# Performance work log

Hardware: AMD Instinct MI355X
Metric: run time of the kernel (lower is better)

The kernel has to match this reference:

```python
import jax, jax.numpy as jnp
import numpy as np

B, S, D, H = 2, 2048, 1024, 16
HD = D // H

def setup_inputs() -> dict:
    key = jax.random.key(0)
    k1, k2, k3 = jax.random.split(key, 3)
    x = jax.random.normal(k1, (B, S, D), dtype=jnp.float32)
    c_attn_w = jax.random.normal(k2, (D, 3 * D), dtype=jnp.float32) * 0.02
    c_attn_b = jnp.zeros((3 * D,), dtype=jnp.float32)
    c_proj_w = jax.random.normal(k3, (D, D), dtype=jnp.float32) * 0.02
    c_proj_b = jnp.zeros((D,), dtype=jnp.float32)
    return {"x": x, "c_attn_w": c_attn_w, "c_attn_b": c_attn_b,
            "c_proj_w": c_proj_w, "c_proj_b": c_proj_b}

def reference(x, c_attn_w, c_attn_b, c_proj_w, c_proj_b):
    bsz, seq_len, d = x.shape
    # Conv1D: addmm(bias, x, weight) -> x @ W + b
    qkv = x @ c_attn_w + c_attn_b                      # [B,S,3D]
    xq, xk, xv = jnp.split(qkv, 3, axis=-1)
    # [B,H,S,hd]
    xq = xq.reshape(bsz, seq_len, H, HD).transpose(0, 2, 1, 3)
    xk = xk.reshape(bsz, seq_len, H, HD).transpose(0, 2, 1, 3)
    xv = xv.reshape(bsz, seq_len, H, HD).transpose(0, 2, 1, 3)
    # Eager attention: QK^T / sqrt(hd), causal mask, softmax, AV
    scale = jnp.asarray(HD, x.dtype) ** 0.5
    attn_weights = jnp.einsum('bhqd,bhkd->bhqk', xq, xk) / scale
    causal = jnp.tril(jnp.ones((seq_len, seq_len), dtype=bool))
    mask_value = jnp.finfo(attn_weights.dtype).min
    attn_weights = jnp.where(causal[None, None], attn_weights, mask_value)
    attn_weights = jax.nn.softmax(attn_weights, axis=-1)
    attn_output = jnp.einsum('bhqk,bhkd->bhqd', attn_weights, xv)  # [B,H,S,hd]
    attn_output = attn_output.transpose(0, 2, 1, 3).reshape(bsz, seq_len, d)
    attn_output = attn_output @ c_proj_w + c_proj_b
    return attn_output
```

## Files before the change

kernel.cpp:

```cpp
#include <hip/hip_runtime.h>
#include <hip/hip_bf16.h>
#include <stdint.h>

#define S_LEN 2048
#define D_DIM 1024
#define N_HEAD 16

typedef unsigned short u16;
typedef __attribute__((ext_vector_type(4))) float f32x4;
typedef __attribute__((ext_vector_type(16))) float f32x16;
typedef __attribute__((ext_vector_type(8))) short bf16x8;
typedef __attribute__((ext_vector_type(4))) unsigned short u16x4;
typedef __attribute__((ext_vector_type(4))) float flt4;

#define MFMA16(a, b, c) __builtin_amdgcn_mfma_f32_16x16x32_bf16((a), (b), (c), 0, 0, 0)
#define MFMA32(a, b, c) __builtin_amdgcn_mfma_f32_32x32x16_bf16((a), (b), (c), 0, 0, 0)

__device__ __forceinline__ u16 f32_bf16(float f) {
    union { float f; uint32_t u; } x;
    x.f = f;
    uint32_t r = (x.u + 0x7FFFu + ((x.u >> 16) & 1u)) >> 16;
    return (u16)r;
}

__device__ __forceinline__ uint32_t pack2(float a, float b) {
    __hip_bfloat162 h = __float22bfloat162_rn(float2{a, b});
    return *(uint32_t*)&h;
}

__device__ __forceinline__ void gload_lds16(const void* g, void* l) {
    __builtin_amdgcn_global_load_lds(
        (const __attribute__((address_space(1))) unsigned int*)(uintptr_t)g,
        (__attribute__((address_space(3))) unsigned int*)(uint32_t)(uintptr_t)l,
        16, 0, 0);
}


__global__ __launch_bounds__(256) void cvt_bf16_kernel(const float* __restrict__ in,
                                                       u16* __restrict__ out, int n) {
    int i = (blockIdx.x * 256 + threadIdx.x) * 4;
    if (i < n) {
        flt4 v = *(const flt4*)(in + i);
        u16x4 u;
        u[0] = f32_bf16(v[0]); u[1] = f32_bf16(v[1]);
        u[2] = f32_bf16(v[2]); u[3] = f32_bf16(v[3]);
        *(u16x4*)(out + i) = u;
    }
}

__global__ __launch_bounds__(256) void transpose_cvt_kernel(const float* __restrict__ in,
                                                            u16* __restrict__ out,
                                                            int R, int C) {
    __shared__ float tile[32][33];
    int tc = blockIdx.x * 32, tr = blockIdx.y * 32;
    int lx = threadIdx.x & 31, ly = threadIdx.x >> 5;
#pragma unroll
    for (int i = 0; i < 32; i += 8)
        tile[ly + i][lx] = in[(size_t)(tr + ly + i) * C + tc + lx];
    __syncthreads();
#pragma unroll
    for (int i = 0; i < 32; i += 8)
        out[(size_t)(tc + ly + i) * R + tr + lx] = f32_bf16(tile[lx][ly + i]);
}


template <int MODE>
__global__ __launch_bounds__(256)
void gemm_bt_kernel(const u16* __restrict__ A, const u16* __restrict__ Bt,
                    const float* __restrict__ bias,
                    float* __restrict__ outF,
                    u16* __restrict__ qo, u16* __restrict__ ko, u16* __restrict__ vto,
                    int M, int N, int K) {
    __shared__ u16 As[128 * 32];
    __shared__ u16 Bs[128 * 32];
    const int tid = threadIdx.x;
    const int w = tid >> 6, lane = tid & 63;
    const int lr = lane & 15, lg = lane >> 4;
    const int bm = blockIdx.y * 128, bn = blockIdx.x * 128;
    const int wr = w >> 1, wc = w & 1;

    f32x4 acc[4][4];
#pragma unroll
    for (int m = 0; m < 4; m++)
#pragma unroll
        for (int n = 0; n < 4; n++) acc[m][n] = (f32x4){0.f, 0.f, 0.f, 0.f};

    const u16* Abase = A + (size_t)(bm + (tid >> 2)) * K + (tid & 3) * 8;
    const u16* Bbase = Bt + (size_t)(bn + (tid >> 2)) * K + (tid & 3) * 8;
    u16* AsW = As + w * 512;
    u16* BsW = Bs + w * 512;

    for (int kt = 0; kt < K; kt += 32) {
        gload_lds16(Abase + kt, AsW);
        gload_lds16(Abase + kt + (size_t)64 * K, AsW + 2048);
        gload_lds16(Bbase + kt, BsW);
        gload_lds16(Bbase + kt + (size_t)64 * K, BsW + 2048);
        __syncthreads();

        bf16x8 a[4], b[4];
        const bf16x8* Av = (const bf16x8*)As;
        const bf16x8* Bv = (const bf16x8*)Bs;
#pragma unroll
        for (int m = 0; m < 4; m++) a[m] = Av[(wr * 64 + m * 16 + lr) * 4 + lg];
#pragma unroll
        for (int n = 0; n < 4; n++) b[n] = Bv[(wc * 64 + n * 16 + lr) * 4 + lg];
#pragma unroll
        for (int m = 0; m < 4; m++)
#pragma unroll
            for (int n = 0; n < 4; n++)
                acc[m][n] = MFMA16(a[m], b[n], acc[m][n]);
        __syncthreads();
    }

    const int rowb = bm + wr * 64, colb = bn + wc * 64;
    if (MODE == 0) {
#pragma unroll
        for (int m = 0; m < 4; m++)
#pragma unroll
            for (int j = 0; j < 4; j++) {
                int r = rowb + m * 16 + lg * 4 + j;
                size_t base = (size_t)r * N;
#pragma unroll
                for (int n = 0; n < 4; n++) {
                    int c = colb + n * 16 + lr;
                    outF[base + c] = acc[m][n][j] + bias[c];
                }
            }
    } else {
#pragma unroll
        for (int m = 0; m < 4; m++)
#pragma unroll
            for (int j = 0; j < 4; j++) {
                int r = rowb + m * 16 + lg * 4 + j;
                int bb = r >> 11, s = r & (S_LEN - 1);
#pragma unroll
                for (int n = 0; n < 4; n++) {
                    int c = colb + n * 16 + lr;
                    float v = acc[m][n][j] + bias[c];
                    int part = c >> 10, cc = c & (D_DIM - 1);
                    if (part == 0) v *= 0.125f * 1.44269504f;
                    u16 bv = f32_bf16(v);
                    int h = cc >> 6, d = cc & 63;
                    size_t bh = (size_t)(bb * N_HEAD + h);
                    if (part == 0)      qo[(bh * S_LEN + s) * 64 + d] = bv;
                    else if (part == 1) ko[(bh * S_LEN + s) * 64 + d] = bv;
                    else                vto[(bh * 64 + d) * S_LEN + s] = bv;
                }
            }
    }
}


__global__ __launch_bounds__(64)
void flash_attn_kernel(const u16* __restrict__ Qg, const u16* __restrict__ Kg,
                       const u16* __restrict__ Vt, u16* __restrict__ Og) {
    const int id = blockIdx.x;
    const int bh = id & 31;
    const int qt = 63 - (id >> 5);
    const int qbase = qt * 32;
    const int lane = threadIdx.x;
    const int ql = lane & 31, hi = lane >> 5;

    const u16* Qh = Qg + (size_t)bh * S_LEN * 64;
    const u16* Kh = Kg + (size_t)bh * S_LEN * 64;
    const u16* Vh = Vt + (size_t)bh * 64 * S_LEN;

    bf16x8 qf[4];
#pragma unroll
    for (int c = 0; c < 4; c++)
        qf[c] = *(const bf16x8*)(Qh + (size_t)(qbase + ql) * 64 + c * 16 + hi * 8);

    f32x16 ot0 = {}, ot1 = {};
    float m = -1e30f, l = 0.f;

    bf16x8 kn[4], vn[4];
#pragma unroll
    for (int c = 0; c < 4; c++)
        kn[c] = *(const bf16x8*)(Kh + (size_t)ql * 64 + c * 16 + hi * 8);
#pragma unroll
    for (int u = 0; u < 4; u++)
        vn[u] = *(const bf16x8*)(Vh + (size_t)((u >> 1) * 32 + ql) * S_LEN + (u & 1) * 16 + hi * 8);

    for (int t = 0; t <= qt; ++t) {
        bf16x8 ka[4] = {kn[0], kn[1], kn[2], kn[3]};
        bf16x8 va[4] = {vn[0], vn[1], vn[2], vn[3]};
        if (t < qt) {
            const size_t kvn = (size_t)(t + 1) * 32;
#pragma unroll
            for (int c = 0; c < 4; c++)
                kn[c] = *(const bf16x8*)(Kh + (kvn + ql) * 64 + c * 16 + hi * 8);
#pragma unroll
            for (int u = 0; u < 4; u++)
                vn[u] = *(const bf16x8*)(Vh + (size_t)((u >> 1) * 32 + ql) * S_LEN + kvn + (u & 1) * 16 + hi * 8);
        }

        f32x16 st = {};
        __builtin_amdgcn_s_setprio(1);
#pragma unroll
        for (int c = 0; c < 4; c++) st = MFMA32(ka[c], qf[c], st);
        __builtin_amdgcn_s_setprio(0);

        float s[16];
#pragma unroll
        for (int r = 0; r < 16; r++) s[r] = st[r];
        if (t == qt) {
#pragma unroll
            for (int r = 0; r < 16; r++) {
                int kvl = ((r & 3) + 8 * (r >> 2)) + 4 * hi;
                if (kvl > ql) s[r] = -1e30f;
            }
        }

        float t0 = fmaxf(s[0], s[1]),   t1 = fmaxf(s[2], s[3]);
        float t2 = fmaxf(s[4], s[5]),   t3 = fmaxf(s[6], s[7]);
        float t4 = fmaxf(s[8], s[9]),   t5 = fmaxf(s[10], s[11]);
        float t6 = fmaxf(s[12], s[13]), t7 = fmaxf(s[14], s[15]);
        t0 = fmaxf(t0, t1); t2 = fmaxf(t2, t3); t4 = fmaxf(t4, t5); t6 = fmaxf(t6, t7);
        float tmax = fmaxf(fmaxf(t0, t2), fmaxf(t4, t6));
        tmax = fmaxf(tmax, __shfl_xor(tmax, 32));

        float corr = 1.f;
        if (!__all(tmax <= m)) {
            float mnew = fmaxf(m, tmax);
            corr = __builtin_amdgcn_exp2f(m - mnew);
            m = mnew;
            ot0 *= corr;
            ot1 *= corr;
        }

        float pe[16];
        float rs = 0.f;
#pragma unroll
        for (int r = 0; r < 16; r++) { pe[r] = __builtin_amdgcn_exp2f(s[r] - m); rs += pe[r]; }
        rs += __shfl_xor(rs, 32);
        l = l * corr + rs;

        uint32_t wv[8];
#pragma unroll
        for (int sp = 0; sp < 8; sp++) wv[sp] = pack2(pe[2 * sp], pe[2 * sp + 1]);
        auto r02 = __builtin_amdgcn_permlane32_swap(wv[0], wv[2], false, false);
        auto r13 = __builtin_amdgcn_permlane32_swap(wv[1], wv[3], false, false);
        auto r46 = __builtin_amdgcn_permlane32_swap(wv[4], wv[6], false, false);
        auto r57 = __builtin_amdgcn_permlane32_swap(wv[5], wv[7], false, false);
        union { uint32_t u[4]; bf16x8 v; } pa0, pa1;
        pa0.u[0] = r02[0]; pa0.u[1] = r13[0]; pa0.u[2] = r02[1]; pa0.u[3] = r13[1];
        pa1.u[0] = r46[0]; pa1.u[1] = r57[0]; pa1.u[2] = r46[1]; pa1.u[3] = r57[1];

        __builtin_amdgcn_s_setprio(1);
        ot0 = MFMA32(va[0], pa0.v, ot0);
        ot0 = MFMA32(va[1], pa1.v, ot0);
        ot1 = MFMA32(va[2], pa0.v, ot1);
        ot1 = MFMA32(va[3], pa1.v, ot1);
        __builtin_amdgcn_s_setprio(0);
    }

    const float inv = 1.f / l;
    const int b = bh >> 4, hh = bh & 15;
    u16* orow = Og + ((size_t)(b * S_LEN) + qbase + ql) * D_DIM + hh * 64;
#pragma unroll
    for (int rp = 0; rp < 8; rp++) {
        const int r = rp * 2;
        const int d = ((r & 3) + 8 * (r >> 2)) + 4 * hi;
        *(uint32_t*)(orow + d) = pack2(ot0[r] * inv, ot0[r + 1] * inv);
        *(uint32_t*)(orow + 32 + d) = pack2(ot1[r] * inv, ot1[r + 1] * inv);
    }
}


extern "C" void kernel_launch(void* const* d_in, const int* in_sizes, int n_in,
                              void* d_out, int out_size, void* d_ws, size_t ws_size,
                              hipStream_t stream) {
    const float* x  = (const float*)d_in[0];
    const float* w1 = (const float*)d_in[1];
    const float* b1 = (const float*)d_in[2];
    const float* w2 = (const float*)d_in[3];
    const float* b2 = (const float*)d_in[4];
    float* out = (float*)d_out;

    u16* ws  = (u16*)d_ws;
    u16* xb  = ws;
    u16* w1t = xb  + 4096 * 1024;
    u16* w2t = w1t + 3072 * 1024;
    u16* q   = w2t + 1024 * 1024;
    u16* k   = q   + 4194304;
    u16* vt  = k   + 4194304;
    u16* x2  = vt  + 4194304;

    cvt_bf16_kernel<<<dim3(4096), dim3(256), 0, stream>>>(x, xb, 4096 * 1024);
    transpose_cvt_kernel<<<dim3(3072 / 32, 1024 / 32), dim3(256), 0, stream>>>(w1, w1t, 1024, 3072);
    transpose_cvt_kernel<<<dim3(1024 / 32, 1024 / 32), dim3(256), 0, stream>>>(w2, w2t, 1024, 1024);

    gemm_bt_kernel<1><<<dim3(3072 / 128, 4096 / 128), dim3(256), 0, stream>>>(
        xb, w1t, b1, nullptr, q, k, vt, 4096, 3072, 1024);

    flash_attn_kernel<<<dim3(2048), dim3(64), 0, stream>>>(q, k, vt, x2);

    gemm_bt_kernel<0><<<dim3(1024 / 128, 4096 / 128), dim3(256), 0, stream>>>(
        x2, w2t, b2, out, nullptr, nullptr, nullptr, 4096, 1024, 1024);
}
```

Measured before the change: 235.1 us.

## Pair causal query tiles per block and split KV range across two waves

The flash attention kernel now gives each block two query tiles (p and 63-p) so every block does the same amount of causal work. Both tiles share each loaded K/V tile. The KV loop is split across two waves, even and odd tiles, and the partial softmax states are merged through shared memory at the end. This aims to fix the load imbalance of the triangular causal workload and halve K/V reloads per query. The cost is more registers per wave, an LDS merge step and a block-wide sync.

Result: faster. 218.5 us (-7.0%).

```diff
diff --git a/kernel.cpp b/kernel.cpp
--- a/kernel.cpp
+++ b/kernel.cpp
@@ -151,66 +151,56 @@
 }
 
 
-__global__ __launch_bounds__(64)
+__global__ __launch_bounds__(128, 2)
 void flash_attn_kernel(const u16* __restrict__ Qg, const u16* __restrict__ Kg,
                        const u16* __restrict__ Vt, u16* __restrict__ Og) {
     const int id = blockIdx.x;
     const int bh = id & 31;
-    const int qt = 63 - (id >> 5);
-    const int qbase = qt * 32;
-    const int lane = threadIdx.x;
+    const int p  = id >> 5;
+    const int w = threadIdx.x >> 6;
+    const int lane = threadIdx.x & 63;
     const int ql = lane & 31, hi = lane >> 5;
+    const int qbA = p * 32, qbB = (63 - p) * 32;
+    const int last = 63 - p;
 
     const u16* Qh = Qg + (size_t)bh * S_LEN * 64;
     const u16* Kh = Kg + (size_t)bh * S_LEN * 64;
     const u16* Vh = Vt + (size_t)bh * 64 * S_LEN;
 
-    bf16x8 qf[4];
-#pragma unroll
-    for (int c = 0; c < 4; c++)
-        qf[c] = *(const bf16x8*)(Qh + (size_t)(qbase + ql) * 64 + c * 16 + hi * 8);
-
-    f32x16 ot0 = {}, ot1 = {};
-    float m = -1e30f, l = 0.f;
-
-    bf16x8 kn[4], vn[4];
-#pragma unroll
-    for (int c = 0; c < 4; c++)
-        kn[c] = *(const bf16x8*)(Kh + (size_t)ql * 64 + c * 16 + hi * 8);
-#pragma unroll
-    for (int u = 0; u < 4; u++)
-        vn[u] = *(const bf16x8*)(Vh + (size_t)((u >> 1) * 32 + ql) * S_LEN + (u & 1) * 16 + hi * 8);
-
-    for (int t = 0; t <= qt; ++t) {
-        bf16x8 ka[4] = {kn[0], kn[1], kn[2], kn[3]};
-        bf16x8 va[4] = {vn[0], vn[1], vn[2], vn[3]};
-        if (t < qt) {
-            const size_t kvn = (size_t)(t + 1) * 32;
-#pragma unroll
-            for (int c = 0; c < 4; c++)
-                kn[c] = *(const bf16x8*)(Kh + (kvn + ql) * 64 + c * 16 + hi * 8);
-#pragma unroll
-            for (int u = 0; u < 4; u++)
-                vn[u] = *(const bf16x8*)(Vh + (size_t)((u >> 1) * 32 + ql) * S_LEN + kvn + (u & 1) * 16 + hi * 8);
-        }
-
-        f32x16 st = {};
-        __builtin_amdgcn_s_setprio(1);
-#pragma unroll
-        for (int c = 0; c < 4; c++) st = MFMA32(ka[c], qf[c], st);
-        __builtin_amdgcn_s_setprio(0);
-
+    __shared__ float mbuf[2][64][34];
+
+    bf16x8 qfA[4], qfB[4];
+#pragma unroll
+    for (int c = 0; c < 4; c++) {
+        qfA[c] = *(const bf16x8*)(Qh + (size_t)(qbA + ql) * 64 + c * 16 + hi * 8);
+        qfB[c] = *(const bf16x8*)(Qh + (size_t)(qbB + ql) * 64 + c * 16 + hi * 8);
+    }
+
+    f32x16 otA0 = {}, otA1 = {}, otB0 = {}, otB1 = {};
+    float mA = -1e30f, lA = 0.f, mB = -1e30f, lB = 0.f;
+
+    auto loadKV = [&](int t, bf16x8 (&k)[4], bf16x8 (&v)[4]) {
+        const u16* kp = Kh + ((size_t)t * 32 + ql) * 64 + hi * 8;
+#pragma unroll
+        for (int c = 0; c < 4; c++) k[c] = *(const bf16x8*)(kp + c * 16);
+        const size_t kv0 = (size_t)t * 32;
+#pragma unroll
+        for (int u = 0; u < 4; u++)
+            v[u] = *(const bf16x8*)(Vh + ((size_t)((u >> 1) * 32 + ql)) * S_LEN + kv0 + (u & 1) * 16 + hi * 8);
+    };
+
+    auto softpv = [&](const f32x16& st, bool diag, float& m, float& l,
+                      f32x16& o0, f32x16& o1, const bf16x8 (&v)[4]) {
         float s[16];
 #pragma unroll
         for (int r = 0; r < 16; r++) s[r] = st[r];
-        if (t == qt) {
+        if (diag) {
 #pragma unroll
             for (int r = 0; r < 16; r++) {
                 int kvl = ((r & 3) + 8 * (r >> 2)) + 4 * hi;
                 if (kvl > ql) s[r] = -1e30f;
             }
         }
-
         float t0 = fmaxf(s[0], s[1]),   t1 = fmaxf(s[2], s[3]);
         float t2 = fmaxf(s[4], s[5]),   t3 = fmaxf(s[6], s[7]);
         float t4 = fmaxf(s[8], s[9]),   t5 = fmaxf(s[10], s[11]);
@@ -221,13 +211,12 @@
 
         float corr = 1.f;
         if (!__all(tmax <= m)) {
-            float mnew = fmaxf(m, tmax);
-            corr = __builtin_amdgcn_exp2f(m - mnew);
-            m = mnew;
-            ot0 *= corr;
-            ot1 *= corr;
+            float mn = fmaxf(m, tmax);
+            corr = __builtin_amdgcn_exp2f(m - mn);
+            m = mn;
+            o0 *= corr;
+            o1 *= corr;
         }
-
         float pe[16];
         float rs = 0.f;
 #pragma unroll
@@ -247,22 +236,78 @@
         pa1.u[0] = r46[0]; pa1.u[1] = r57[0]; pa1.u[2] = r46[1]; pa1.u[3] = r57[1];
 
         __builtin_amdgcn_s_setprio(1);
-        ot0 = MFMA32(va[0], pa0.v, ot0);
-        ot0 = MFMA32(va[1], pa1.v, ot0);
-        ot1 = MFMA32(va[2], pa0.v, ot1);
-        ot1 = MFMA32(va[3], pa1.v, ot1);
+        o0 = MFMA32(v[0], pa0.v, o0);
+        o0 = MFMA32(v[1], pa1.v, o0);
+        o1 = MFMA32(v[2], pa0.v, o1);
+        o1 = MFMA32(v[3], pa1.v, o1);
         __builtin_amdgcn_s_setprio(0);
-    }
-
-    const float inv = 1.f / l;
-    const int b = bh >> 4, hh = bh & 15;
-    u16* orow = Og + ((size_t)(b * S_LEN) + qbase + ql) * D_DIM + hh * 64;
-#pragma unroll
-    for (int rp = 0; rp < 8; rp++) {
-        const int r = rp * 2;
-        const int d = ((r & 3) + 8 * (r >> 2)) + 4 * hi;
-        *(uint32_t*)(orow + d) = pack2(ot0[r] * inv, ot0[r + 1] * inv);
-        *(uint32_t*)(orow + 32 + d) = pack2(ot1[r] * inv, ot1[r + 1] * inv);
+    };
+
+    auto step = [&](int t, const bf16x8 (&k)[4], const bf16x8 (&v)[4]) {
+        const bool actA = (t <= p);
+        f32x16 stA = {}, stB = {};
+        __builtin_amdgcn_s_setprio(1);
+        if (actA) {
+#pragma unroll
+            for (int c = 0; c < 4; c++) stA = MFMA32(k[c], qfA[c], stA);
+        }
+#pragma unroll
+        for (int c = 0; c < 4; c++) stB = MFMA32(k[c], qfB[c], stB);
+        __builtin_amdgcn_s_setprio(0);
+        if (actA) softpv(stA, t == p, mA, lA, otA0, otA1, v);
+        softpv(stB, t == last, mB, lB, otB0, otB1, v);
+    };
+
+    bf16x8 k0[4], v0[4], k1[4], v1[4];
+    loadKV(w, k0, v0);
+    int t = w;
+    for (;;) {
+        if (t + 2 <= last) loadKV(t + 2, k1, v1);
+        step(t, k0, v0);
+        t += 2;
+        if (t > last) break;
+        if (t + 2 <= last) loadKV(t + 2, k0, v0);
+        step(t, k1, v1);
+        t += 2;
+        if (t > last) break;
+    }
+
+    if (w == 1) {
+        float* bA = mbuf[0][lane];
+        float* bB = mbuf[1][lane];
+        bA[0] = mA; bA[1] = lA;
+        bB[0] = mB; bB[1] = lB;
+#pragma unroll
+        for (int r = 0; r < 16; r++) {
+            bA[2 + r] = otA0[r]; bA[18 + r] = otA1[r];
+            bB[2 + r] = otB0[r]; bB[18 + r] = otB1[r];
+        }
+    }
+    __syncthreads();
+    if (w == 0) {
+        const int bb = bh >> 4, hh = bh & 15;
+        auto fin = [&](float m0, float l0, const f32x16& o0, const f32x16& o1,
+                       const float* b, int qbase) {
+            float m1 = b[0], l1 = b[1];
+            float ms = fmaxf(m0, m1);
+            float a0 = __builtin_amdgcn_exp2f(m0 - ms);
+            float a1 = __builtin_amdgcn_exp2f(m1 - ms);
+            float inv = 1.f / (l0 * a0 + l1 * a1);
+            u16* orow = Og + ((size_t)(bb * S_LEN) + qbase + ql) * D_DIM + hh * 64;
+#pragma unroll
+            for (int rp = 0; rp < 8; rp++) {
+                int r = rp * 2;
+                int d = ((r & 3) + 8 * (r >> 2)) + 4 * hi;
+                float x0 = (o0[r] * a0 + b[2 + r] * a1) * inv;
+                float x1 = (o0[r + 1] * a0 + b[2 + r + 1] * a1) * inv;
+                *(uint32_t*)(orow + d) = pack2(x0, x1);
+                float y0 = (o1[r] * a0 + b[18 + r] * a1) * inv;
+                float y1 = (o1[r + 1] * a0 + b[18 + r + 1] * a1) * inv;
+                *(uint32_t*)(orow + 32 + d) = pack2(y0, y1);
+            }
+        };
+        fin(mA, lA, otA0, otA1, mbuf[0][lane], qbA);
+        fin(mB, lB, otB0, otB1, mbuf[1][lane], qbB);
     }
 }
 
@@ -293,7 +338,7 @@
     gemm_bt_kernel<1><<<dim3(3072 / 128, 4096 / 128), dim3(256), 0, stream>>>(
         xb, w1t, b1, nullptr, q, k, vt, 4096, 3072, 1024);
 
-    flash_attn_kernel<<<dim3(2048), dim3(64), 0, stream>>>(q, k, vt, x2);
+    flash_attn_kernel<<<dim3(1024), dim3(128), 0, stream>>>(q, k, vt, x2);
 
     gemm_bt_kernel<0><<<dim3(1024 / 128, 4096 / 128), dim3(256), 0, stream>>>(
         x2, w2t, b2, out, nullptr, nullptr, nullptr, 4096, 1024, 1024);
```
